# Kernel tuning notes

Hardware: AMD Instinct MI355X
Metric: run time of the kernel (lower is better)

## Reference

```python
import jax, jax.numpy as jnp
import numpy as np

GRID_SIZE = 8
SPLINE_ORDER = 3
LAYERS = [256, 512, 512, 256]  # [input_dim] + hidden_dims
BATCH = 8192
BN_EPS = 1e-5


def make_grid(in_features):
    # efficient-kan/torchkan grid: uniform on [-1, 1] extended by spline_order on each side
    h = 2.0 / GRID_SIZE
    g = jnp.arange(-SPLINE_ORDER, GRID_SIZE + SPLINE_ORDER + 1, dtype=jnp.float32) * h - 1.0
    return jnp.broadcast_to(g, (in_features, g.shape[0]))  # (In, G + 2k + 1)


def b_splines(x, grid):
    # x: (B, In), grid: (In, G + 2k + 1) -> bases: (B, In, G + k)
    xg = x[:, :, None]
    bases = ((xg >= grid[:, :-1]) & (xg < grid[:, 1:])).astype(x.dtype)
    for k in range(1, SPLINE_ORDER + 1):
        left = (xg - grid[:, : -(k + 1)]) / (grid[:, k:-1] - grid[:, : -(k + 1)])
        right = (grid[:, k + 1 :] - xg) / (grid[:, k + 1 :] - grid[:, 1:-k])
        bases = left * bases[:, :, :-1] + right * bases[:, :, 1:]
    return bases


def kan_linear(x, grid, base_w, spline_w):
    # base path: GELU (exact, matching torch.nn.GELU) then linear
    base_out = jax.nn.gelu(x, approximate=False) @ base_w.T
    spline_out = jnp.einsum('bik,oik->bo', b_splines(x, grid), spline_w)
    return base_out + spline_out


def setup_inputs() -> dict:
    key = jax.random.key(0)
    ks = jax.random.split(key, 16)
    inp = {'x': jax.random.normal(ks[0], (BATCH, LAYERS[0]), dtype=jnp.float32)}
    n_bases = GRID_SIZE + SPLINE_ORDER
    for i, (fin, fout) in enumerate(zip(LAYERS[:-1], LAYERS[1:])):
        scale = 1.0 / np.sqrt(fin)
        inp[f'grid{i}'] = make_grid(fin)
        inp[f'base_w{i}'] = jax.random.normal(ks[1 + 3 * i], (fout, fin), dtype=jnp.float32) * scale
        inp[f'spline_w{i}'] = jax.random.normal(ks[2 + 3 * i], (fout, fin, n_bases), dtype=jnp.float32) * (0.1 * scale)
    d_out = LAYERS[-1]
    inp['bn_gamma'] = jnp.ones((d_out,), dtype=jnp.float32)
    inp['bn_beta'] = jnp.zeros((d_out,), dtype=jnp.float32)
    inp['bn_mean'] = jax.random.normal(ks[10], (d_out,), dtype=jnp.float32) * 0.1
    inp['bn_var'] = jax.random.uniform(ks[11], (d_out,), dtype=jnp.float32, minval=0.5, maxval=1.5)
    return inp


def reference(x, grid0, base_w0, spline_w0, grid1, base_w1, spline_w1, grid2, base_w2, spline_w2, bn_gamma, bn_beta, bn_mean, bn_var):
    h = kan_linear(x, grid0, base_w0, spline_w0)
    h = kan_linear(h, grid1, base_w1, spline_w1)
    h = kan_linear(h, grid2, base_w2, spline_w2)
    # BatchNorm1d in eval mode (running stats); Dropout is identity at inference
    return bn_gamma * (h - bn_mean) * jax.lax.rsqrt(bn_var + BN_EPS) + bn_beta
```

## Files before the change

### kernel.cpp

```cpp
#include <hip/hip_runtime.h>
#include <hip/hip_bf16.h>
#include <cstdint>


typedef unsigned short ushort_t;
typedef __bf16 bf16x8 __attribute__((ext_vector_type(8)));
typedef float f32x4 __attribute__((ext_vector_type(4)));
typedef _Float16 f16x2 __attribute__((ext_vector_type(2)));
typedef _Float16 f16x4 __attribute__((ext_vector_type(4)));

__device__ __forceinline__ ushort_t f2bf(float f) {
    __bf16 h = (__bf16)f;
    return __builtin_bit_cast(ushort_t, h);
}

__device__ __forceinline__ void gload_lds16(const void* g, void* lds) {
    __builtin_amdgcn_global_load_lds(
        (const __attribute__((address_space(1))) unsigned int*)(uintptr_t)g,
        (__attribute__((address_space(3))) unsigned int*)(unsigned int)(uintptr_t)lds,
        16, 0, 0);
}

__device__ __forceinline__ void expand12(float x, ushort_t* o) {
    float x3 = x * x * x;
    float y  = 0.7978845608028654f * (x + 0.044715f * x3);
    float e  = __expf(2.0f * y);
    float th = 1.0f - 2.0f / (e + 1.0f);
    o[0] = f2bf(0.5f * x * (1.0f + th));
    float xs = (x + 1.75f) * 4.0f;
#pragma unroll
    for (int j = 0; j < 11; ++j) {
        float t  = xs - (float)j;
        float a  = fabsf(t - 2.0f);
        float p1 = (3.0f * a - 6.0f) * a * a + 4.0f;
        float c  = 2.0f - a;
        float p2 = c * c * c;
        float v  = (a <= 1.0f) ? p1 : fmaxf(p2, 0.0f);
        o[1 + j] = f2bf(v * (1.0f / 6.0f));
    }
}

__global__ __launch_bounds__(256) void expand_kernel(
    const float* __restrict__ X0, ushort_t* __restrict__ A, int total2)
{
    int idx = blockIdx.x * 256 + threadIdx.x;
    if (idx >= total2) return;
    float2 h = *(const float2*)(X0 + 2 * (size_t)idx);
    union { ushort_t us[24]; uint4 v[3]; } pk;
    expand12(h.x, pk.us);
    expand12(h.y, pk.us + 12);
    uint4* dst = (uint4*)(A + (size_t)idx * 24);
    dst[0] = pk.v[0]; dst[1] = pk.v[1]; dst[2] = pk.v[2];
}

__global__ __launch_bounds__(256) void expand_sum_kernel(
    const _Float16* __restrict__ P, size_t pstride,
    ushort_t* __restrict__ A, int total2)
{
    int idx = blockIdx.x * 256 + threadIdx.x;
    if (idx >= total2) return;
    float hx = 0.f, hy = 0.f;
#pragma unroll
    for (int s = 0; s < 4; ++s) {
        f16x2 v = *(const f16x2*)(P + s * pstride + 2 * (size_t)idx);
        hx += (float)v.x; hy += (float)v.y;
    }
    union { ushort_t us[24]; uint4 v[3]; } pk;
    expand12(hx, pk.us);
    expand12(hy, pk.us + 12);
    uint4* dst = (uint4*)(A + (size_t)idx * 24);
    dst[0] = pk.v[0]; dst[1] = pk.v[1]; dst[2] = pk.v[2];
}

__global__ __launch_bounds__(256) void pack_w_kernel(
    const float* __restrict__ bw, const float* __restrict__ sw,
    ushort_t* __restrict__ W, int total)
{
    int idx = blockIdx.x * 256 + threadIdx.x;
    if (idx >= total) return;
    union { ushort_t us[12]; uint2 v[3]; } pk;
    pk.us[0] = f2bf(bw[idx]);
    const float* s = sw + (size_t)idx * 11;
#pragma unroll
    for (int k = 0; k < 11; ++k) pk.us[1 + k] = f2bf(s[k]);
    uint2* dst = (uint2*)(W + (size_t)idx * 12);
    dst[0] = pk.v[0]; dst[1] = pk.v[1]; dst[2] = pk.v[2];
}

#define SLOTE 16384

__global__ __launch_bounds__(512, 2) void gemm_kernel(
    const ushort_t* __restrict__ A,
    const ushort_t* __restrict__ W,
    _Float16* __restrict__ C,
    int M, int N, int K, int scps)
{
    extern __shared__ __align__(16) ushort_t lds[];

    const int t   = threadIdx.x;
    const int l   = t & 63;
    const int w   = t >> 6;
    const int wm  = w >> 2;
    const int wn  = w & 3;
    const int l15 = l & 15;
    const int q   = l >> 4;
    const int blockM = blockIdx.x * 256;
    const int blockN = blockIdx.y * 256;
    const int kb0 = blockIdx.z * scps;
    const int nt  = scps;
    _Float16* Cz = C + (size_t)blockIdx.z * M * N;

    const ushort_t* Ab = A + (size_t)blockM * K;
    const ushort_t* Wb = W + (size_t)blockN * K;

    auto stage = [&](int kb, int slot) {
        ushort_t* da = lds + slot * SLOTE;
        ushort_t* db = da + 8192;
#pragma unroll
        for (int it = 0; it < 2; ++it) {
            int s = it * 512 + t;
            int row = s >> 2, c = s & 3, g = c ^ (row & 3);
            gload_lds16(Ab + ((size_t)row * K + (kb << 5) + g * 8), da + s * 8);
        }
#pragma unroll
        for (int it = 0; it < 2; ++it) {
            int s = it * 512 + t;
            int row = s >> 2, c = s & 3, g = c ^ (row & 3);
            gload_lds16(Wb + ((size_t)row * K + (kb << 5) + g * 8), db + s * 8);
        }
    };

    f32x4 acc[8][4];
#pragma unroll
    for (int i = 0; i < 8; ++i)
#pragma unroll
        for (int j = 0; j < 4; ++j) acc[i][j] = (f32x4){0.f, 0.f, 0.f, 0.f};

    stage(kb0 + 0, 0); stage(kb0 + 1, 1); stage(kb0 + 2, 2);
    asm volatile("s_waitcnt vmcnt(8)" ::: "memory");
    __builtin_amdgcn_s_barrier();

    for (int tt = 0; tt < nt; ++tt) {
        const int slot = tt & 3;
        const ushort_t* Ac = lds + slot * SLOTE;
        const ushort_t* Bc = Ac + 8192;

        if (tt + 3 < nt) stage(kb0 + tt + 3, (tt + 3) & 3);

        bf16x8 bfr[4], afr[8];
#pragma unroll
        for (int ni = 0; ni < 4; ++ni) {
            int n = wn * 64 + ni * 16 + l15;
            bfr[ni] = *(const bf16x8*)&Bc[(size_t)((n << 2) + (q ^ (n & 3))) * 8];
        }
#pragma unroll
        for (int mi = 0; mi < 8; ++mi) {
            int m = wm * 128 + mi * 16 + l15;
            afr[mi] = *(const bf16x8*)&Ac[(size_t)((m << 2) + (q ^ (m & 3))) * 8];
        }

        asm volatile("s_waitcnt lgkmcnt(7)" ::: "memory");
        __builtin_amdgcn_sched_barrier(0);
        __builtin_amdgcn_s_setprio(1);
#pragma unroll
        for (int ni = 0; ni < 4; ++ni)
            acc[0][ni] = __builtin_amdgcn_mfma_f32_16x16x32_bf16(
                afr[0], bfr[ni], acc[0][ni], 0, 0, 0);

        asm volatile("s_waitcnt lgkmcnt(4)" ::: "memory");
        __builtin_amdgcn_sched_barrier(0);
#pragma unroll
        for (int mi = 1; mi < 4; ++mi)
#pragma unroll
            for (int ni = 0; ni < 4; ++ni)
                acc[mi][ni] = __builtin_amdgcn_mfma_f32_16x16x32_bf16(
                    afr[mi], bfr[ni], acc[mi][ni], 0, 0, 0);

        asm volatile("s_waitcnt lgkmcnt(0)" ::: "memory");
        __builtin_amdgcn_sched_barrier(0);
#pragma unroll
        for (int mi = 4; mi < 8; ++mi)
#pragma unroll
            for (int ni = 0; ni < 4; ++ni)
                acc[mi][ni] = __builtin_amdgcn_mfma_f32_16x16x32_bf16(
                    afr[mi], bfr[ni], acc[mi][ni], 0, 0, 0);
        __builtin_amdgcn_s_setprio(0);

        if (tt + 3 < nt)      asm volatile("s_waitcnt vmcnt(8)" ::: "memory");
        else if (tt + 2 < nt) asm volatile("s_waitcnt vmcnt(4)" ::: "memory");
        else if (tt + 1 < nt) asm volatile("s_waitcnt vmcnt(0)" ::: "memory");
        __builtin_amdgcn_s_barrier();
    }

#pragma unroll
    for (int ni = 0; ni < 4; ++ni) {
        int n = blockN + wn * 64 + ni * 16 + l15;
#pragma unroll
        for (int mi = 0; mi < 8; ++mi) {
            int mb = blockM + wm * 128 + mi * 16 + q * 4;
#pragma unroll
            for (int r = 0; r < 4; ++r)
                Cz[(size_t)(mb + r) * N + n] = (_Float16)acc[mi][ni][r];
        }
    }
}

__global__ __launch_bounds__(256) void bn_reduce_kernel(
    const _Float16* __restrict__ Q, size_t qstride,
    const float* __restrict__ gamma, const float* __restrict__ beta,
    const float* __restrict__ mean,  const float* __restrict__ var,
    float4* __restrict__ out, int n4)
{
    int i = blockIdx.x * 256 + threadIdx.x;
    if (i >= n4) return;
    float sx = 0.f, sy = 0.f, sz = 0.f, sw = 0.f;
#pragma unroll
    for (int s = 0; s < 8; ++s) {
        f16x4 v = *(const f16x4*)(Q + s * qstride + 4 * (size_t)i);
        sx += (float)v.x; sy += (float)v.y; sz += (float)v.z; sw += (float)v.w;
    }
    int nb = (i * 4) & 255;
    float4 g  = *(const float4*)(gamma + nb);
    float4 be = *(const float4*)(beta + nb);
    float4 mn = *(const float4*)(mean + nb);
    float4 vr = *(const float4*)(var + nb);
    float4 o;
    o.x = g.x * rsqrtf(vr.x + 1e-5f) * (sx - mn.x) + be.x;
    o.y = g.y * rsqrtf(vr.y + 1e-5f) * (sy - mn.y) + be.y;
    o.z = g.z * rsqrtf(vr.z + 1e-5f) * (sz - mn.z) + be.z;
    o.w = g.w * rsqrtf(vr.w + 1e-5f) * (sw - mn.w) + be.w;
    out[i] = o;
}

extern "C" void kernel_launch(void* const* d_in, const int* in_sizes, int n_in,
                              void* d_out, int out_size, void* d_ws, size_t ws_size,
                              hipStream_t stream) {
    const float* x     = (const float*)d_in[0];
    const float* bw0   = (const float*)d_in[2];
    const float* sw0   = (const float*)d_in[3];
    const float* bw1   = (const float*)d_in[5];
    const float* sw1   = (const float*)d_in[6];
    const float* bw2   = (const float*)d_in[8];
    const float* sw2   = (const float*)d_in[9];
    const float* gamma = (const float*)d_in[10];
    const float* beta  = (const float*)d_in[11];
    const float* mean  = (const float*)d_in[12];
    const float* var   = (const float*)d_in[13];

    char* ws = (char*)d_ws;
    ushort_t*  Abuf = (ushort_t*)(ws);
    ushort_t*  W0   = (ushort_t*)(ws + 100663296);
    ushort_t*  W1   = (ushort_t*)(ws + 103809024);
    ushort_t*  W2   = (ushort_t*)(ws + 110100480);
    _Float16*  P    = (_Float16*)(ws + 113246208);
    float*     out  = (float*)d_out;

    const size_t PS01 = (size_t)8192 * 512;
    const size_t PS2  = (size_t)8192 * 256;
    const size_t GEMM_LDS = 4 * SLOTE * sizeof(ushort_t);

    pack_w_kernel<<<(512 * 256 + 255) / 256, 256, 0, stream>>>(bw0, sw0, W0, 512 * 256);
    pack_w_kernel<<<(512 * 512 + 255) / 256, 256, 0, stream>>>(bw1, sw1, W1, 512 * 512);
    pack_w_kernel<<<(256 * 512 + 255) / 256, 256, 0, stream>>>(bw2, sw2, W2, 256 * 512);

    expand_kernel<<<4096, 256, 0, stream>>>(x, Abuf, 8192 * 256 / 2);
    {
        dim3 g(32, 2, 4);
        gemm_kernel<<<g, 512, GEMM_LDS, stream>>>(Abuf, W0, P, 8192, 512, 3072, 24);
    }
    expand_sum_kernel<<<8192, 256, 0, stream>>>(P, PS01, Abuf, 8192 * 512 / 2);
    {
        dim3 g(32, 2, 4);
        gemm_kernel<<<g, 512, GEMM_LDS, stream>>>(Abuf, W1, P, 8192, 512, 6144, 48);
    }
    expand_sum_kernel<<<8192, 256, 0, stream>>>(P, PS01, Abuf, 8192 * 512 / 2);
    {
        dim3 g(32, 1, 8);
        gemm_kernel<<<g, 512, GEMM_LDS, stream>>>(Abuf, W2, P, 8192, 256, 6144, 24);
    }
    bn_reduce_kernel<<<2048, 256, 0, stream>>>(
        P, PS2, gamma, beta, mean, var, (float4*)out, 8192 * 256 / 4);
}
```

Baseline: 311.1 us.

## Double-buffer GEMM register fragments, change LDS swizzle, widen expand_sum per thread

```diff
diff --git a/kernel.cpp b/kernel.cpp
--- a/kernel.cpp
+++ b/kernel.cpp
@@ -6,7 +6,6 @@
 typedef unsigned short ushort_t;
 typedef __bf16 bf16x8 __attribute__((ext_vector_type(8)));
 typedef float f32x4 __attribute__((ext_vector_type(4)));
-typedef _Float16 f16x2 __attribute__((ext_vector_type(2)));
 typedef _Float16 f16x4 __attribute__((ext_vector_type(4)));
 
 __device__ __forceinline__ ushort_t f2bf(float f) {
@@ -55,21 +54,24 @@
 
 __global__ __launch_bounds__(256) void expand_sum_kernel(
     const _Float16* __restrict__ P, size_t pstride,
-    ushort_t* __restrict__ A, int total2)
+    ushort_t* __restrict__ A, int total4)
 {
     int idx = blockIdx.x * 256 + threadIdx.x;
-    if (idx >= total2) return;
-    float hx = 0.f, hy = 0.f;
+    if (idx >= total4) return;
+    float h0 = 0.f, h1 = 0.f, h2 = 0.f, h3 = 0.f;
 #pragma unroll
     for (int s = 0; s < 4; ++s) {
-        f16x2 v = *(const f16x2*)(P + s * pstride + 2 * (size_t)idx);
-        hx += (float)v.x; hy += (float)v.y;
-    }
-    union { ushort_t us[24]; uint4 v[3]; } pk;
-    expand12(hx, pk.us);
-    expand12(hy, pk.us + 12);
-    uint4* dst = (uint4*)(A + (size_t)idx * 24);
-    dst[0] = pk.v[0]; dst[1] = pk.v[1]; dst[2] = pk.v[2];
+        f16x4 v = *(const f16x4*)(P + s * pstride + 4 * (size_t)idx);
+        h0 += (float)v.x; h1 += (float)v.y; h2 += (float)v.z; h3 += (float)v.w;
+    }
+    union { ushort_t us[48]; uint4 v[6]; } pk;
+    expand12(h0, pk.us);
+    expand12(h1, pk.us + 12);
+    expand12(h2, pk.us + 24);
+    expand12(h3, pk.us + 36);
+    uint4* dst = (uint4*)(A + (size_t)idx * 48);
+#pragma unroll
+    for (int i = 0; i < 6; ++i) dst[i] = pk.v[i];
 }
 
 __global__ __launch_bounds__(256) void pack_w_kernel(
@@ -119,77 +121,67 @@
 #pragma unroll
         for (int it = 0; it < 2; ++it) {
             int s = it * 512 + t;
-            int row = s >> 2, c = s & 3, g = c ^ (row & 3);
+            int row = s >> 2, g = (s & 3) ^ ((row >> 1) & 3);
             gload_lds16(Ab + ((size_t)row * K + (kb << 5) + g * 8), da + s * 8);
         }
 #pragma unroll
         for (int it = 0; it < 2; ++it) {
             int s = it * 512 + t;
-            int row = s >> 2, c = s & 3, g = c ^ (row & 3);
+            int row = s >> 2, g = (s & 3) ^ ((row >> 1) & 3);
             gload_lds16(Wb + ((size_t)row * K + (kb << 5) + g * 8), db + s * 8);
         }
     };
 
-    f32x4 acc[8][4];
-#pragma unroll
-    for (int i = 0; i < 8; ++i)
-#pragma unroll
-        for (int j = 0; j < 4; ++j) acc[i][j] = (f32x4){0.f, 0.f, 0.f, 0.f};
-
-    stage(kb0 + 0, 0); stage(kb0 + 1, 1); stage(kb0 + 2, 2);
-    asm volatile("s_waitcnt vmcnt(8)" ::: "memory");
-    __builtin_amdgcn_s_barrier();
-
-    for (int tt = 0; tt < nt; ++tt) {
-        const int slot = tt & 3;
+    auto ldfrags = [&](int slot, bf16x8* afr, bf16x8* bfr) {
         const ushort_t* Ac = lds + slot * SLOTE;
         const ushort_t* Bc = Ac + 8192;
-
-        if (tt + 3 < nt) stage(kb0 + tt + 3, (tt + 3) & 3);
-
-        bf16x8 bfr[4], afr[8];
 #pragma unroll
         for (int ni = 0; ni < 4; ++ni) {
             int n = wn * 64 + ni * 16 + l15;
-            bfr[ni] = *(const bf16x8*)&Bc[(size_t)((n << 2) + (q ^ (n & 3))) * 8];
+            bfr[ni] = *(const bf16x8*)&Bc[(size_t)((n << 2) + (q ^ ((n >> 1) & 3))) * 8];
         }
 #pragma unroll
         for (int mi = 0; mi < 8; ++mi) {
             int m = wm * 128 + mi * 16 + l15;
-            afr[mi] = *(const bf16x8*)&Ac[(size_t)((m << 2) + (q ^ (m & 3))) * 8];
-        }
-
-        asm volatile("s_waitcnt lgkmcnt(7)" ::: "memory");
+            afr[mi] = *(const bf16x8*)&Ac[(size_t)((m << 2) + (q ^ ((m >> 1) & 3))) * 8];
+        }
+    };
+
+    f32x4 acc[8][4];
+#pragma unroll
+    for (int i = 0; i < 8; ++i)
+#pragma unroll
+        for (int j = 0; j < 4; ++j) acc[i][j] = (f32x4){0.f, 0.f, 0.f, 0.f};
+
+    stage(kb0 + 0, 0); stage(kb0 + 1, 1); stage(kb0 + 2, 2);
+    asm volatile("s_waitcnt vmcnt(4)" ::: "memory");
+    __builtin_amdgcn_s_barrier();
+
+    bf16x8 aA[8], bA[4], aB[8], bB[4];
+    ldfrags(0, aA, bA);
+    asm volatile("s_waitcnt lgkmcnt(0)" ::: "memory");
+
+    auto body = [&](int tt, bf16x8* ac, bf16x8* bc, bf16x8* an, bf16x8* bn) {
+        if (tt + 3 < nt) stage(kb0 + tt + 3, (tt + 3) & 3);
+        if (tt + 1 < nt) ldfrags((tt + 1) & 3, an, bn);
         __builtin_amdgcn_sched_barrier(0);
         __builtin_amdgcn_s_setprio(1);
 #pragma unroll
-        for (int ni = 0; ni < 4; ++ni)
-            acc[0][ni] = __builtin_amdgcn_mfma_f32_16x16x32_bf16(
-                afr[0], bfr[ni], acc[0][ni], 0, 0, 0);
-
-        asm volatile("s_waitcnt lgkmcnt(4)" ::: "memory");
-        __builtin_amdgcn_sched_barrier(0);
-#pragma unroll
-        for (int mi = 1; mi < 4; ++mi)
+        for (int mi = 0; mi < 8; ++mi)
 #pragma unroll
             for (int ni = 0; ni < 4; ++ni)
                 acc[mi][ni] = __builtin_amdgcn_mfma_f32_16x16x32_bf16(
-                    afr[mi], bfr[ni], acc[mi][ni], 0, 0, 0);
-
+                    ac[mi], bc[ni], acc[mi][ni], 0, 0, 0);
+        __builtin_amdgcn_s_setprio(0);
         asm volatile("s_waitcnt lgkmcnt(0)" ::: "memory");
-        __builtin_amdgcn_sched_barrier(0);
-#pragma unroll
-        for (int mi = 4; mi < 8; ++mi)
-#pragma unroll
-            for (int ni = 0; ni < 4; ++ni)
-                acc[mi][ni] = __builtin_amdgcn_mfma_f32_16x16x32_bf16(
-                    afr[mi], bfr[ni], acc[mi][ni], 0, 0, 0);
-        __builtin_amdgcn_s_setprio(0);
-
-        if (tt + 3 < nt)      asm volatile("s_waitcnt vmcnt(8)" ::: "memory");
-        else if (tt + 2 < nt) asm volatile("s_waitcnt vmcnt(4)" ::: "memory");
-        else if (tt + 1 < nt) asm volatile("s_waitcnt vmcnt(0)" ::: "memory");
+        if (tt + 3 < nt)      asm volatile("s_waitcnt vmcnt(4)" ::: "memory");
+        else if (tt + 2 < nt) asm volatile("s_waitcnt vmcnt(0)" ::: "memory");
         __builtin_amdgcn_s_barrier();
+    };
+
+    for (int tt = 0; tt < nt; tt += 2) {
+        body(tt,     aA, bA, aB, bB);
+        body(tt + 1, aB, bB, aA, bA);
     }
 
 #pragma unroll
@@ -268,12 +260,12 @@
         dim3 g(32, 2, 4);
         gemm_kernel<<<g, 512, GEMM_LDS, stream>>>(Abuf, W0, P, 8192, 512, 3072, 24);
     }
-    expand_sum_kernel<<<8192, 256, 0, stream>>>(P, PS01, Abuf, 8192 * 512 / 2);
+    expand_sum_kernel<<<4096, 256, 0, stream>>>(P, PS01, Abuf, 8192 * 512 / 4);
     {
         dim3 g(32, 2, 4);
         gemm_kernel<<<g, 512, GEMM_LDS, stream>>>(Abuf, W1, P, 8192, 512, 6144, 48);
     }
-    expand_sum_kernel<<<8192, 256, 0, stream>>>(P, PS01, Abuf, 8192 * 512 / 2);
+    expand_sum_kernel<<<4096, 256, 0, stream>>>(P, PS01, Abuf, 8192 * 512 / 4);
     {
         dim3 g(32, 1, 8);
         gemm_kernel<<<g, 512, GEMM_LDS, stream>>>(Abuf, W2, P, 8192, 256, 6144, 24);
```

Result: slower. 326.3 us (+4.9%).
